# Performance work log

Hardware: AMD Instinct MI355X
Metric: run time of the kernel (lower is better)

The kernel has to match this reference:

```python
import jax, jax.numpy as jnp
import numpy as np

N_ROUTING_ITERS = 10


def setup_inputs() -> dict:
    key = jax.random.key(0)
    k1, k2, k3 = jax.random.split(key, 3)
    b, in_caps, in_ch, out_ch = 64, 1152, 512, 512
    input_x = jax.random.normal(k1, (b, in_caps, in_ch), dtype=jnp.float32)
    # nn.Linear(in_ch, out_ch): weight [out, in] -> store transposed [in, out]
    lim = 1.0 / np.sqrt(in_ch)
    W = jax.random.uniform(k2, (in_ch, out_ch), minval=-lim, maxval=lim, dtype=jnp.float32)
    bias = jax.random.uniform(k3, (out_ch,), minval=-lim, maxval=lim, dtype=jnp.float32)
    coeffs = jnp.ones((1, in_caps, 1), dtype=jnp.float32)
    return {"input_x": input_x, "W": W, "bias": bias, "coeffs": coeffs}


def _squash(sj):
    # squash over channel dim: x * ||x||^2 / ((1+||x||^2) * ||x||) = x * ||x|| / (1+||x||^2)
    norm = jnp.linalg.norm(sj, axis=-1, keepdims=True)
    return sj * norm / (1.0 + norm * norm)


def reference(input_x, W, bias, coeffs):
    # u_ji: [b, in_caps, out_ch]
    u = jnp.einsum('bic,co->bio', input_x, W) + bias

    def step(c, _):
        cij = jax.nn.softmax(c, axis=1)                      # [1, in_caps, 1]
        sj = jnp.sum(u * cij, axis=1, keepdims=True)         # [b, 1, out]
        vj = _squash(sj).squeeze(1)                          # [b, out]
        upd = jnp.einsum('bio,bo->i', u, vj)                 # agreement, summed over batch
        return c + upd[None, :, None], vj

    _, vjs = jax.lax.scan(step, coeffs, None, length=N_ROUTING_ITERS)
    return vjs[-1]
```

## Files before the change

### kernel.cpp

```cpp
#include <hip/hip_runtime.h>
#include <cstddef>

#define B      64
#define IC     1152
#define CH     512
#define SPLITS 16


__device__ __forceinline__ float waveReduceSum(float v) {
    #pragma unroll
    for (int o = 32; o; o >>= 1) v += __shfl_down(v, o, 64);
    return v;
}
__device__ __forceinline__ float waveReduceMax(float v) {
    #pragma unroll
    for (int o = 32; o; o >>= 1) v = fmaxf(v, __shfl_down(v, o, 64));
    return v;
}

template<int NT>
__device__ __forceinline__ float blockReduceSum(float v, float* red) {
    __syncthreads();
    const int lane = threadIdx.x & 63, w = threadIdx.x >> 6;
    v = waveReduceSum(v);
    if (lane == 0) red[w] = v;
    __syncthreads();
    if (threadIdx.x == 0) {
        float t = red[0];
        #pragma unroll
        for (int k = 1; k < NT / 64; ++k) t += red[k];
        red[0] = t;
    }
    __syncthreads();
    return red[0];
}

template<int NT>
__device__ __forceinline__ float blockReduceMax(float v, float* red) {
    __syncthreads();
    const int lane = threadIdx.x & 63, w = threadIdx.x >> 6;
    v = waveReduceMax(v);
    if (lane == 0) red[w] = v;
    __syncthreads();
    if (threadIdx.x == 0) {
        float t = red[0];
        #pragma unroll
        for (int k = 1; k < NT / 64; ++k) t = fmaxf(t, red[k]);
        red[0] = t;
    }
    __syncthreads();
    return red[0];
}


__global__ __launch_bounds__(1024) void k_transpose(const float* __restrict__ W,
                                                    float* __restrict__ WT) {
    __shared__ float tile[32][33];
    int x = blockIdx.x * 32 + threadIdx.x;
    int y = blockIdx.y * 32 + threadIdx.y;
    tile[threadIdx.y][threadIdx.x] = W[(size_t)y * CH + x];
    __syncthreads();
    int tx = blockIdx.y * 32 + threadIdx.x;
    int ty = blockIdx.x * 32 + threadIdx.y;
    WT[(size_t)ty * CH + tx] = tile[threadIdx.x][threadIdx.y];
}

__global__ __launch_bounds__(256) void k_wwt(const float* __restrict__ W,
                                             const float* __restrict__ WT,
                                             float* __restrict__ WWT) {
    __shared__ float wa[2][CH];
    const int a0 = blockIdx.x * 2;
    for (int j = threadIdx.x; j < CH; j += 256) {
        wa[0][j] = W[(size_t)a0 * CH + j];
        wa[1][j] = W[(size_t)(a0 + 1) * CH + j];
    }
    __syncthreads();
    const int c0 = threadIdx.x, c1 = threadIdx.x + 256;
    float a00 = 0, a01 = 0, a10 = 0, a11 = 0;
    for (int j = 0; j < CH; ++j) {
        float w0 = wa[0][j], w1 = wa[1][j];
        float t0 = WT[(size_t)j * CH + c0], t1 = WT[(size_t)j * CH + c1];
        a00 += w0 * t0; a01 += w0 * t1;
        a10 += w1 * t0; a11 += w1 * t1;
    }
    WWT[(size_t)a0 * CH + c0] = a00;
    WWT[(size_t)a0 * CH + c1] = a01;
    WWT[(size_t)(a0 + 1) * CH + c0] = a10;
    WWT[(size_t)(a0 + 1) * CH + c1] = a11;
}

__global__ __launch_bounds__(512) void k_wb(const float* __restrict__ WT,
                                            const float* __restrict__ bias,
                                            float* __restrict__ Wb,
                                            float* __restrict__ bb) {
    __shared__ float bS[CH];
    __shared__ float red[8];
    const int c = threadIdx.x;
    bS[c] = bias[c];
    __syncthreads();
    float acc = 0;
    for (int j = 0; j < CH; ++j) acc += bS[j] * WT[(size_t)j * CH + c];
    Wb[c] = acc;
    float n2 = blockReduceSum<512>(bS[c] * bS[c], red);
    if (c == 0) *bb = n2;
}

__global__ void k_init(const float* __restrict__ coeffs, float* __restrict__ cvec) {
    int i = blockIdx.x * 256 + threadIdx.x;
    if (i < IC) cvec[i] = coeffs[i];
}


__global__ __launch_bounds__(256) void k_passA(const float* __restrict__ x,
                                               const float* __restrict__ cvec,
                                               float* __restrict__ xcpart) {
    __shared__ float eS[IC];
    __shared__ float red[4];
    const int b = blockIdx.x, is = blockIdx.y;
    const int t = threadIdx.x;

    float cl[5];
    float m = -3.4e38f;
    #pragma unroll
    for (int k = 0; k < 5; ++k) {
        int i = t + k * 256;
        cl[k] = (i < IC) ? cvec[i] : -3.4e38f;
        m = fmaxf(m, cl[k]);
    }
    float M = blockReduceMax<256>(m, red);
    float z = 0;
    #pragma unroll
    for (int k = 0; k < 5; ++k) {
        int i = t + k * 256;
        if (i < IC) { float e = expf(cl[k] - M); eS[i] = e; z += e; }
    }
    float Z = blockReduceSum<256>(z, red);
    const float invZ = 1.0f / Z;

    const int i0 = is * (IC / SPLITS);
    float2 acc = make_float2(0.f, 0.f);
    const float2* xp = reinterpret_cast<const float2*>(x + ((size_t)b * IC + i0) * CH) + t;
    #pragma unroll 4
    for (int i = i0; i < i0 + IC / SPLITS; ++i) {
        float w = eS[i];
        float2 xv = *xp;
        acc.x += w * xv.x;
        acc.y += w * xv.y;
        xp += CH / 2;
    }
    float2* outp = reinterpret_cast<float2*>(xcpart + ((size_t)(is * B + b)) * CH) + t;
    *outp = make_float2(acc.x * invZ, acc.y * invZ);
}

__global__ __launch_bounds__(1024) void k_core(const float* __restrict__ xcpart,
                                               const float* __restrict__ WWT,
                                               const float* __restrict__ Wb,
                                               const float* __restrict__ bbp,
                                               float* __restrict__ Wv) {
    __shared__ float xcS[CH];
    __shared__ float hS[CH];
    __shared__ float red[16];
    __shared__ float gS;
    const int b = blockIdx.x, tid = threadIdx.x;
    const int c = tid & (CH - 1), half = tid >> 9;

    if (half == 0) {
        float s = 0;
        #pragma unroll
        for (int is = 0; is < SPLITS; ++is) s += xcpart[((size_t)(is * B + b)) * CH + c];
        xcS[c] = s;
    }
    __syncthreads();

    float acc = 0;
    const int cp0 = half * (CH / 2);
    for (int cp = cp0; cp < cp0 + CH / 2; ++cp)
        acc += xcS[cp] * WWT[(size_t)cp * CH + c];
    if (half == 0) hS[c] = acc;
    __syncthreads();
    if (half == 1) hS[c] += acc;
    __syncthreads();

    float part = 0;
    if (half == 0) {
        float xcv = xcS[c];
        part = xcv * hS[c] + 2.0f * Wb[c] * xcv;
    }
    float tot = blockReduceSum<1024>(part, red);
    if (tid == 0) {
        float n2 = tot + *bbp;
        float n = sqrtf(n2);
        gS = n / (1.0f + n2);
    }
    __syncthreads();
    if (half == 0) Wv[(size_t)b * CH + c] = gS * (hS[c] + Wb[c]);
}

__global__ __launch_bounds__(256) void k_passC(const float* __restrict__ x,
                                               const float* __restrict__ Wv,
                                               float* __restrict__ cvec) {
    __shared__ float red[4];
    const int i = blockIdx.x, t = threadIdx.x;
    float acc = 0;
    const float2* wvp = reinterpret_cast<const float2*>(Wv) + t;
    const float2* xp = reinterpret_cast<const float2*>(x) + (size_t)i * (CH / 2) + t;
    #pragma unroll 4
    for (int b = 0; b < B; ++b) {
        float2 xv = xp[(size_t)b * IC * (CH / 2)];
        float2 wv = wvp[(size_t)b * (CH / 2)];
        acc += xv.x * wv.x + xv.y * wv.y;
    }
    float tot = blockReduceSum<256>(acc, red);
    if (t == 0) cvec[i] += tot;
}

__global__ __launch_bounds__(512) void k_final(const float* __restrict__ xcpart,
                                               const float* __restrict__ W,
                                               const float* __restrict__ bias,
                                               float* __restrict__ out) {
    __shared__ float xcS[CH];
    __shared__ float red[8];
    __shared__ float gS;
    const int b = blockIdx.x, j = threadIdx.x;
    float s = 0;
    #pragma unroll
    for (int is = 0; is < SPLITS; ++is) s += xcpart[((size_t)(is * B + b)) * CH + j];
    xcS[j] = s;
    __syncthreads();
    float sj = bias[j];
    for (int c = 0; c < CH; ++c) sj += xcS[c] * W[(size_t)c * CH + j];
    float n2 = blockReduceSum<512>(sj * sj, red);
    if (j == 0) { float n = sqrtf(n2); gS = n / (1.0f + n2); }
    __syncthreads();
    out[(size_t)b * CH + j] = sj * gS;
}


extern "C" void kernel_launch(void* const* d_in, const int* in_sizes, int n_in,
                              void* d_out, int out_size, void* d_ws, size_t ws_size,
                              hipStream_t stream) {
    (void)in_sizes; (void)n_in; (void)out_size; (void)ws_size;
    const float* x      = (const float*)d_in[0];
    const float* W      = (const float*)d_in[1];
    const float* bias   = (const float*)d_in[2];
    const float* coeffs = (const float*)d_in[3];
    float* out = (float*)d_out;
    float* ws  = (float*)d_ws;

    float* WT     = ws;
    float* WWT    = ws + 262144;
    float* Wb     = ws + 524288;
    float* bb     = ws + 524800;
    float* cvec   = ws + 524816;
    float* Wv     = ws + 525968;
    float* xcpart = ws + 558736;

    k_transpose<<<dim3(16, 16), dim3(32, 32), 0, stream>>>(W, WT);
    k_wwt<<<256, 256, 0, stream>>>(W, WT, WWT);
    k_wb<<<1, 512, 0, stream>>>(WT, bias, Wb, bb);
    k_init<<<5, 256, 0, stream>>>(coeffs, cvec);

    for (int t = 0; t < 9; ++t) {
        k_passA<<<dim3(B, SPLITS), 256, 0, stream>>>(x, cvec, xcpart);
        k_core<<<B, 1024, 0, stream>>>(xcpart, WWT, Wb, bb, Wv);
        k_passC<<<IC, 256, 0, stream>>>(x, Wv, cvec);
    }
    k_passA<<<dim3(B, SPLITS), 256, 0, stream>>>(x, cvec, xcpart);
    k_final<<<B, 512, 0, stream>>>(xcpart, W, bias, out);
}
```

Baseline: 1.275 ms.

## Convert input to bf16 once and stream it in routing passes

```diff
diff --git a/kernel.cpp b/kernel.cpp
--- a/kernel.cpp
+++ b/kernel.cpp
@@ -52,6 +52,30 @@
     return red[0];
 }
 
+__device__ __forceinline__ unsigned bfpack2(float a, float b) {
+    unsigned ua = __float_as_uint(a), ub = __float_as_uint(b);
+    ua = (ua + 0x7FFFu + ((ua >> 16) & 1u)) >> 16;
+    ub = (ub + 0x7FFFu + ((ub >> 16) & 1u)) & 0xFFFF0000u;
+    return ua | ub;
+}
+__device__ __forceinline__ void bfunpack2(unsigned u, float& lo, float& hi) {
+    lo = __uint_as_float(u << 16);
+    hi = __uint_as_float(u & 0xFFFF0000u);
+}
+
+
+__global__ __launch_bounds__(1024) void k_cvt(const float* __restrict__ x,
+                                              uint4* __restrict__ xbf) {
+    const size_t idx = (size_t)blockIdx.x * 1024 + threadIdx.x;
+    const float4* xp = reinterpret_cast<const float4*>(x) + idx * 2;
+    float4 a = xp[0], b = xp[1];
+    uint4 o;
+    o.x = bfpack2(a.x, a.y);
+    o.y = bfpack2(a.z, a.w);
+    o.z = bfpack2(b.x, b.y);
+    o.w = bfpack2(b.z, b.w);
+    xbf[idx] = o;
+}
 
 __global__ __launch_bounds__(1024) void k_transpose(const float* __restrict__ W,
                                                     float* __restrict__ WT) {
@@ -111,10 +135,11 @@
 }
 
 
-__global__ __launch_bounds__(256) void k_passA(const float* __restrict__ x,
+__global__ __launch_bounds__(256) void k_passA(const uint4* __restrict__ xbf,
                                                const float* __restrict__ cvec,
                                                float* __restrict__ xcpart) {
     __shared__ float eS[IC];
+    __shared__ float accS[3][CH];
     __shared__ float red[4];
     const int b = blockIdx.x, is = blockIdx.y;
     const int t = threadIdx.x;
@@ -137,19 +162,42 @@
     float Z = blockReduceSum<256>(z, red);
     const float invZ = 1.0f / Z;
 
+    const int rp = t >> 6;
+    const int c8 = t & 63;
     const int i0 = is * (IC / SPLITS);
-    float2 acc = make_float2(0.f, 0.f);
-    const float2* xp = reinterpret_cast<const float2*>(x + ((size_t)b * IC + i0) * CH) + t;
-    #pragma unroll 4
-    for (int i = i0; i < i0 + IC / SPLITS; ++i) {
-        float w = eS[i];
-        float2 xv = *xp;
-        acc.x += w * xv.x;
-        acc.y += w * xv.y;
-        xp += CH / 2;
-    }
-    float2* outp = reinterpret_cast<float2*>(xcpart + ((size_t)(is * B + b)) * CH) + t;
-    *outp = make_float2(acc.x * invZ, acc.y * invZ);
+
+    float acc[8];
+    #pragma unroll
+    for (int e = 0; e < 8; ++e) acc[e] = 0.f;
+
+    const uint4* xp = xbf + ((size_t)(b * IC + i0 + rp) * (CH / 8)) + c8;
+    #pragma unroll 2
+    for (int k = 0; k < IC / SPLITS / 4; ++k) {
+        float w = eS[i0 + rp + 4 * k];
+        uint4 u = xp[(size_t)k * 4 * (CH / 8)];
+        float f0, f1;
+        bfunpack2(u.x, f0, f1); acc[0] += w * f0; acc[1] += w * f1;
+        bfunpack2(u.y, f0, f1); acc[2] += w * f0; acc[3] += w * f1;
+        bfunpack2(u.z, f0, f1); acc[4] += w * f0; acc[5] += w * f1;
+        bfunpack2(u.w, f0, f1); acc[6] += w * f0; acc[7] += w * f1;
+    }
+    if (rp > 0) {
+        #pragma unroll
+        for (int e = 0; e < 8; ++e) accS[rp - 1][c8 * 8 + e] = acc[e];
+    }
+    __syncthreads();
+    if (rp == 0) {
+        float4 o0, o1;
+        #pragma unroll
+        for (int e = 0; e < 8; ++e) {
+            float v = acc[e] + accS[0][c8 * 8 + e] + accS[1][c8 * 8 + e] + accS[2][c8 * 8 + e];
+            if (e < 4) reinterpret_cast<float*>(&o0)[e] = v * invZ;
+            else       reinterpret_cast<float*>(&o1)[e - 4] = v * invZ;
+        }
+        float4* outp = reinterpret_cast<float4*>(xcpart + ((size_t)(is * B + b)) * CH) + c8 * 2;
+        outp[0] = o0;
+        outp[1] = o1;
+    }
 }
 
 __global__ __launch_bounds__(1024) void k_core(const float* __restrict__ xcpart,
@@ -196,9 +244,76 @@
     if (half == 0) Wv[(size_t)b * CH + c] = gS * (hS[c] + Wb[c]);
 }
 
-__global__ __launch_bounds__(256) void k_passC(const float* __restrict__ x,
+__global__ __launch_bounds__(256) void k_passC(const uint4* __restrict__ xbf,
                                                const float* __restrict__ Wv,
                                                float* __restrict__ cvec) {
+    __shared__ float red[4];
+    const int i = blockIdx.x, t = threadIdx.x;
+    const int bp = t >> 6;
+    const int c8 = t & 63;
+
+    float acc = 0;
+    #pragma unroll 2
+    for (int k = 0; k < B / 4; ++k) {
+        int b = bp + 4 * k;
+        uint4 u = xbf[((size_t)(b * IC + i)) * (CH / 8) + c8];
+        const float4* wvp = reinterpret_cast<const float4*>(Wv + (size_t)b * CH) + c8 * 2;
+        float4 w0 = wvp[0], w1 = wvp[1];
+        float f0, f1;
+        bfunpack2(u.x, f0, f1); acc += f0 * w0.x + f1 * w0.y;
+        bfunpack2(u.y, f0, f1); acc += f0 * w0.z + f1 * w0.w;
+        bfunpack2(u.z, f0, f1); acc += f0 * w1.x + f1 * w1.y;
+        bfunpack2(u.w, f0, f1); acc += f0 * w1.z + f1 * w1.w;
+    }
+    float tot = blockReduceSum<256>(acc, red);
+    if (t == 0) cvec[i] += tot;
+}
+
+
+__global__ __launch_bounds__(256) void k_passA_f32(const float* __restrict__ x,
+                                                   const float* __restrict__ cvec,
+                                                   float* __restrict__ xcpart) {
+    __shared__ float eS[IC];
+    __shared__ float red[4];
+    const int b = blockIdx.x, is = blockIdx.y;
+    const int t = threadIdx.x;
+
+    float cl[5];
+    float m = -3.4e38f;
+    #pragma unroll
+    for (int k = 0; k < 5; ++k) {
+        int i = t + k * 256;
+        cl[k] = (i < IC) ? cvec[i] : -3.4e38f;
+        m = fmaxf(m, cl[k]);
+    }
+    float M = blockReduceMax<256>(m, red);
+    float z = 0;
+    #pragma unroll
+    for (int k = 0; k < 5; ++k) {
+        int i = t + k * 256;
+        if (i < IC) { float e = expf(cl[k] - M); eS[i] = e; z += e; }
+    }
+    float Z = blockReduceSum<256>(z, red);
+    const float invZ = 1.0f / Z;
+
+    const int i0 = is * (IC / SPLITS);
+    float2 acc = make_float2(0.f, 0.f);
+    const float2* xp = reinterpret_cast<const float2*>(x + ((size_t)b * IC + i0) * CH) + t;
+    #pragma unroll 4
+    for (int i = i0; i < i0 + IC / SPLITS; ++i) {
+        float w = eS[i];
+        float2 xv = *xp;
+        acc.x += w * xv.x;
+        acc.y += w * xv.y;
+        xp += CH / 2;
+    }
+    float2* outp = reinterpret_cast<float2*>(xcpart + ((size_t)(is * B + b)) * CH) + t;
+    *outp = make_float2(acc.x * invZ, acc.y * invZ);
+}
+
+__global__ __launch_bounds__(256) void k_passC_f32(const float* __restrict__ x,
+                                                   const float* __restrict__ Wv,
+                                                   float* __restrict__ cvec) {
     __shared__ float red[4];
     const int i = blockIdx.x, t = threadIdx.x;
     float acc = 0;
@@ -239,13 +354,19 @@
 extern "C" void kernel_launch(void* const* d_in, const int* in_sizes, int n_in,
                               void* d_out, int out_size, void* d_ws, size_t ws_size,
                               hipStream_t stream) {
-    (void)in_sizes; (void)n_in; (void)out_size; (void)ws_size;
+    (void)in_sizes; (void)n_in; (void)out_size;
     const float* x      = (const float*)d_in[0];
     const float* W      = (const float*)d_in[1];
     const float* bias   = (const float*)d_in[2];
     const float* coeffs = (const float*)d_in[3];
     float* out = (float*)d_out;
-    float* ws  = (float*)d_ws;
+
+    const size_t xbf_bytes  = (size_t)B * IC * CH * 2;
+    const size_t f32_floats = 1083024;
+    const bool fast = ws_size >= xbf_bytes + f32_floats * 4 + 256;
+
+    uint4* xbf = (uint4*)d_ws;
+    float* ws  = fast ? (float*)((char*)d_ws + xbf_bytes) : (float*)d_ws;
 
     float* WT     = ws;
     float* WWT    = ws + 262144;
@@ -255,16 +376,27 @@
     float* Wv     = ws + 525968;
     float* xcpart = ws + 558736;
 
+    if (fast)
+        k_cvt<<<(B * IC * CH / 8) / 1024, 1024, 0, stream>>>(x, xbf);
     k_transpose<<<dim3(16, 16), dim3(32, 32), 0, stream>>>(W, WT);
     k_wwt<<<256, 256, 0, stream>>>(W, WT, WWT);
     k_wb<<<1, 512, 0, stream>>>(WT, bias, Wb, bb);
     k_init<<<5, 256, 0, stream>>>(coeffs, cvec);
 
     for (int t = 0; t < 9; ++t) {
-        k_passA<<<dim3(B, SPLITS), 256, 0, stream>>>(x, cvec, xcpart);
-        k_core<<<B, 1024, 0, stream>>>(xcpart, WWT, Wb, bb, Wv);
-        k_passC<<<IC, 256, 0, stream>>>(x, Wv, cvec);
-    }
-    k_passA<<<dim3(B, SPLITS), 256, 0, stream>>>(x, cvec, xcpart);
+        if (fast) {
+            k_passA<<<dim3(B, SPLITS), 256, 0, stream>>>(xbf, cvec, xcpart);
+            k_core<<<B, 1024, 0, stream>>>(xcpart, WWT, Wb, bb, Wv);
+            k_passC<<<IC, 256, 0, stream>>>(xbf, Wv, cvec);
+        } else {
+            k_passA_f32<<<dim3(B, SPLITS), 256, 0, stream>>>(x, cvec, xcpart);
+            k_core<<<B, 1024, 0, stream>>>(xcpart, WWT, Wb, bb, Wv);
+            k_passC_f32<<<IC, 256, 0, stream>>>(x, Wv, cvec);
+        }
+    }
+    if (fast)
+        k_passA<<<dim3(B, SPLITS), 256, 0, stream>>>(xbf, cvec, xcpart);
+    else
+        k_passA_f32<<<dim3(B, SPLITS), 256, 0, stream>>>(x, cvec, xcpart);
     k_final<<<B, 512, 0, stream>>>(xcpart, W, bias, out);
 }
```

After: 1.117 ms. -12.4%, faster.

## Fuse routing iteration into one kernel over a bf16 copy of x

Applied to the files above, without the earlier changes.

```diff
diff --git a/kernel.cpp b/kernel.cpp
--- a/kernel.cpp
+++ b/kernel.cpp
@@ -4,7 +4,7 @@
 #define B      64
 #define IC     1152
 #define CH     512
-#define SPLITS 16
+#define NCVT   2048
 
 
 __device__ __forceinline__ float waveReduceSum(float v) {
@@ -18,7 +18,7 @@
     return v;
 }
 
-template<int NT>
+template<int NTT>
 __device__ __forceinline__ float blockReduceSum(float v, float* red) {
     __syncthreads();
     const int lane = threadIdx.x & 63, w = threadIdx.x >> 6;
@@ -28,14 +28,14 @@
     if (threadIdx.x == 0) {
         float t = red[0];
         #pragma unroll
-        for (int k = 1; k < NT / 64; ++k) t += red[k];
+        for (int k = 1; k < NTT / 64; ++k) t += red[k];
         red[0] = t;
     }
     __syncthreads();
     return red[0];
 }
 
-template<int NT>
+template<int NTT>
 __device__ __forceinline__ float blockReduceMax(float v, float* red) {
     __syncthreads();
     const int lane = threadIdx.x & 63, w = threadIdx.x >> 6;
@@ -45,13 +45,260 @@
     if (threadIdx.x == 0) {
         float t = red[0];
         #pragma unroll
-        for (int k = 1; k < NT / 64; ++k) t = fmaxf(t, red[k]);
+        for (int k = 1; k < NTT / 64; ++k) t = fmaxf(t, red[k]);
         red[0] = t;
     }
     __syncthreads();
     return red[0];
 }
 
+__device__ __forceinline__ unsigned bfpack2(float a, float b) {
+    unsigned ua = __float_as_uint(a), ub = __float_as_uint(b);
+    ua = (ua + 0x7FFFu + ((ua >> 16) & 1u)) >> 16;
+    ub = (ub + 0x7FFFu + ((ub >> 16) & 1u)) & 0xFFFF0000u;
+    return ua | ub;
+}
+__device__ __forceinline__ void bfunpack2(unsigned u, float& lo, float& hi) {
+    lo = __uint_as_float(u << 16);
+    hi = __uint_as_float(u & 0xFFFF0000u);
+}
+
+
+__global__ __launch_bounds__(256) void k_setup(
+    const float* __restrict__ x, const float* __restrict__ W,
+    const float* __restrict__ bias, const float* __restrict__ coeffs,
+    uint4* __restrict__ xbf, float* __restrict__ WWT, float* __restrict__ Wb,
+    float* __restrict__ bb, float* __restrict__ bufs)
+{
+    __shared__ float red[4];
+    const int bid = blockIdx.x, tid = threadIdx.x;
+
+    if (bid < NCVT) {
+        const size_t base = (size_t)bid * (256 * 9) + tid;
+        const float4* xp4 = reinterpret_cast<const float4*>(x);
+        #pragma unroll 3
+        for (int k = 0; k < 9; ++k) {
+            size_t idx = base + (size_t)k * 256;
+            float4 a = xp4[idx * 2], b2 = xp4[idx * 2 + 1];
+            uint4 o;
+            o.x = bfpack2(a.x, a.y); o.y = bfpack2(a.z, a.w);
+            o.z = bfpack2(b2.x, b2.y); o.w = bfpack2(b2.z, b2.w);
+            xbf[idx] = o;
+        }
+    } else if (bid < NCVT + 1024) {
+        const int bidw = bid - NCVT;
+        const int ta = bidw >> 5, tc = bidw & 31;
+        const int a = ta * 16 + (tid >> 4), c2 = tc * 16 + (tid & 15);
+        const float* ra = W + (size_t)a * CH;
+        const float* rc = W + (size_t)c2 * CH;
+        float s = 0;
+        for (int j = 0; j < CH; ++j) s += ra[j] * rc[j];
+        WWT[(size_t)a * CH + c2] = s;
+    } else if (bid == NCVT + 1024) {
+        #pragma unroll
+        for (int r = 0; r < 2; ++r) {
+            int c = tid + r * 256;
+            const float* rw = W + (size_t)c * CH;
+            float s = 0;
+            for (int j = 0; j < CH; ++j) s += rw[j] * bias[j];
+            Wb[c] = s;
+        }
+    } else if (bid == NCVT + 1025) {
+        float v0 = bias[tid], v1 = bias[tid + 256];
+        float n2 = blockReduceSum<256>(v0 * v0 + v1 * v1, red);
+        if (tid == 0) *bb = n2;
+    } else {
+        for (int i = tid; i < IC; i += 256) bufs[i] = coeffs[i];
+        for (int k = tid; k < 9 * IC; k += 256) bufs[IC + k] = 0.f;
+    }
+}
+
+
+__global__ __launch_bounds__(1024) void k_iter(
+    const uint4* __restrict__ xbf, const float* __restrict__ WWT,
+    const float* __restrict__ Wb, const float* __restrict__ bbp,
+    const float* __restrict__ cin, float* __restrict__ cout)
+{
+    __shared__ float eS[IC];
+    __shared__ float accS[15][CH];
+    __shared__ float xcS[CH];
+    __shared__ float hS[CH];
+    __shared__ float WvS[CH];
+    __shared__ float red[16];
+    __shared__ float gS;
+    const int b = blockIdx.x, tid = threadIdx.x;
+
+    float c0v = cin[tid];
+    float c1v = (tid < IC - 1024) ? cin[tid + 1024] : -3.4e38f;
+    float M = blockReduceMax<1024>(fmaxf(c0v, c1v), red);
+    float e0 = expf(c0v - M);
+    float e1 = (tid < IC - 1024) ? expf(c1v - M) : 0.f;
+    eS[tid] = e0;
+    if (tid < IC - 1024) eS[tid + 1024] = e1;
+    float Z = blockReduceSum<1024>(e0 + e1, red);
+    const float invZ = 1.0f / Z;
+
+    const int rp = tid >> 6;
+    const int c8 = tid & 63;
+    float acc[8];
+    #pragma unroll
+    for (int e = 0; e < 8; ++e) acc[e] = 0.f;
+    {
+        const uint4* xp = xbf + ((size_t)b * IC + rp) * (CH / 8) + c8;
+        for (int i = rp; i < IC; i += 16) {
+            float w = eS[i];
+            uint4 u = *xp; xp += 16 * (CH / 8);
+            float f0, f1;
+            bfunpack2(u.x, f0, f1); acc[0] += w * f0; acc[1] += w * f1;
+            bfunpack2(u.y, f0, f1); acc[2] += w * f0; acc[3] += w * f1;
+            bfunpack2(u.z, f0, f1); acc[4] += w * f0; acc[5] += w * f1;
+            bfunpack2(u.w, f0, f1); acc[6] += w * f0; acc[7] += w * f1;
+        }
+    }
+    if (rp > 0) {
+        #pragma unroll
+        for (int e = 0; e < 8; ++e) accS[rp - 1][c8 * 8 + e] = acc[e];
+    }
+    __syncthreads();
+    if (rp == 0) {
+        #pragma unroll
+        for (int e = 0; e < 8; ++e) {
+            float v = acc[e];
+            #pragma unroll
+            for (int k = 0; k < 15; ++k) v += accS[k][c8 * 8 + e];
+            xcS[c8 * 8 + e] = v * invZ;
+        }
+    }
+    __syncthreads();
+
+    const int cc = tid & (CH - 1), half = tid >> 9;
+    float hp = 0;
+    {
+        const int cp0 = half * (CH / 2);
+        for (int cp = cp0; cp < cp0 + CH / 2; ++cp)
+            hp += xcS[cp] * WWT[(size_t)cp * CH + cc];
+    }
+    if (half == 1) hS[cc] = hp;
+    __syncthreads();
+    float part = 0;
+    if (half == 0) {
+        float h = hp + hS[cc];
+        hS[cc] = h;
+        float xv = xcS[cc];
+        part = xv * h + 2.0f * Wb[cc] * xv;
+    }
+    float tot = blockReduceSum<1024>(part, red);
+    if (tid == 0) {
+        float n2 = tot + *bbp;
+        float n = sqrtf(n2);
+        gS = n / (1.0f + n2);
+    }
+    __syncthreads();
+    if (half == 0) WvS[cc] = gS * (hS[cc] + Wb[cc]);
+    __syncthreads();
+
+    {
+        const float4* wv4 = reinterpret_cast<const float4*>(WvS) + c8 * 2;
+        float4 w0 = wv4[0], w1 = wv4[1];
+        const uint4* xq = xbf + ((size_t)b * IC + rp) * (CH / 8) + c8;
+        for (int i = rp; i < IC; i += 16) {
+            uint4 u = *xq; xq += 16 * (CH / 8);
+            float f0, f1, s = 0;
+            bfunpack2(u.x, f0, f1); s += f0 * w0.x + f1 * w0.y;
+            bfunpack2(u.y, f0, f1); s += f0 * w0.z + f1 * w0.w;
+            bfunpack2(u.z, f0, f1); s += f0 * w1.x + f1 * w1.y;
+            bfunpack2(u.w, f0, f1); s += f0 * w1.z + f1 * w1.w;
+            s = waveReduceSum(s);
+            if (c8 == 0) atomicAdd(cout + i, s);
+        }
+    }
+    if (b == 0) {
+        for (int i = tid; i < IC; i += 1024) atomicAdd(cout + i, cin[i]);
+    }
+}
+
+
+__global__ __launch_bounds__(1024) void k_final(
+    const uint4* __restrict__ xbf, const float* __restrict__ W,
+    const float* __restrict__ bias, const float* __restrict__ cin,
+    float* __restrict__ out)
+{
+    __shared__ float eS[IC];
+    __shared__ float accS[15][CH];
+    __shared__ float xcS[CH];
+    __shared__ float hS[CH];
+    __shared__ float red[16];
+    __shared__ float gS;
+    const int b = blockIdx.x, tid = threadIdx.x;
+
+    float c0v = cin[tid];
+    float c1v = (tid < IC - 1024) ? cin[tid + 1024] : -3.4e38f;
+    float M = blockReduceMax<1024>(fmaxf(c0v, c1v), red);
+    float e0 = expf(c0v - M);
+    float e1 = (tid < IC - 1024) ? expf(c1v - M) : 0.f;
+    eS[tid] = e0;
+    if (tid < IC - 1024) eS[tid + 1024] = e1;
+    float Z = blockReduceSum<1024>(e0 + e1, red);
+    const float invZ = 1.0f / Z;
+
+    const int rp = tid >> 6, c8 = tid & 63;
+    float acc[8];
+    #pragma unroll
+    for (int e = 0; e < 8; ++e) acc[e] = 0.f;
+    {
+        const uint4* xp = xbf + ((size_t)b * IC + rp) * (CH / 8) + c8;
+        for (int i = rp; i < IC; i += 16) {
+            float w = eS[i];
+            uint4 u = *xp; xp += 16 * (CH / 8);
+            float f0, f1;
+            bfunpack2(u.x, f0, f1); acc[0] += w * f0; acc[1] += w * f1;
+            bfunpack2(u.y, f0, f1); acc[2] += w * f0; acc[3] += w * f1;
+            bfunpack2(u.z, f0, f1); acc[4] += w * f0; acc[5] += w * f1;
+            bfunpack2(u.w, f0, f1); acc[6] += w * f0; acc[7] += w * f1;
+        }
+    }
+    if (rp > 0) {
+        #pragma unroll
+        for (int e = 0; e < 8; ++e) accS[rp - 1][c8 * 8 + e] = acc[e];
+    }
+    __syncthreads();
+    if (rp == 0) {
+        #pragma unroll
+        for (int e = 0; e < 8; ++e) {
+            float v = acc[e];
+            #pragma unroll
+            for (int k = 0; k < 15; ++k) v += accS[k][c8 * 8 + e];
+            xcS[c8 * 8 + e] = v * invZ;
+        }
+    }
+    __syncthreads();
+
+    const int j = tid & (CH - 1), half = tid >> 9;
+    float sp = 0;
+    {
+        const int cp0 = half * (CH / 2);
+        for (int cp = cp0; cp < cp0 + CH / 2; ++cp)
+            sp += xcS[cp] * W[(size_t)cp * CH + j];
+    }
+    if (half == 1) hS[j] = sp;
+    __syncthreads();
+    float part = 0;
+    if (half == 0) {
+        float s = sp + hS[j] + bias[j];
+        hS[j] = s;
+        part = s * s;
+    }
+    float tot = blockReduceSum<1024>(part, red);
+    if (tid == 0) {
+        float n = sqrtf(tot);
+        gS = n / (1.0f + tot);
+    }
+    __syncthreads();
+    if (half == 0) out[(size_t)b * CH + j] = hS[j] * gS;
+}
+
+
+#define SPLITS 16
 
 __global__ __launch_bounds__(1024) void k_transpose(const float* __restrict__ W,
                                                     float* __restrict__ WT) {
@@ -65,9 +312,9 @@
     WT[(size_t)ty * CH + tx] = tile[threadIdx.x][threadIdx.y];
 }
 
-__global__ __launch_bounds__(256) void k_wwt(const float* __restrict__ W,
-                                             const float* __restrict__ WT,
-                                             float* __restrict__ WWT) {
+__global__ __launch_bounds__(256) void k_wwt_f(const float* __restrict__ W,
+                                               const float* __restrict__ WT,
+                                               float* __restrict__ WWT) {
     __shared__ float wa[2][CH];
     const int a0 = blockIdx.x * 2;
     for (int j = threadIdx.x; j < CH; j += 256) {
@@ -89,10 +336,10 @@
     WWT[(size_t)(a0 + 1) * CH + c1] = a11;
 }
 
-__global__ __launch_bounds__(512) void k_wb(const float* __restrict__ WT,
-                                            const float* __restrict__ bias,
-                                            float* __restrict__ Wb,
-                                            float* __restrict__ bb) {
+__global__ __launch_bounds__(512) void k_wb_f(const float* __restrict__ WT,
+                                              const float* __restrict__ bias,
+                                              float* __restrict__ Wb,
+                                              float* __restrict__ bb) {
     __shared__ float bS[CH];
     __shared__ float red[8];
     const int c = threadIdx.x;
@@ -105,20 +352,18 @@
     if (c == 0) *bb = n2;
 }
 
-__global__ void k_init(const float* __restrict__ coeffs, float* __restrict__ cvec) {
+__global__ void k_init_f(const float* __restrict__ coeffs, float* __restrict__ cvec) {
     int i = blockIdx.x * 256 + threadIdx.x;
     if (i < IC) cvec[i] = coeffs[i];
 }
 
-
-__global__ __launch_bounds__(256) void k_passA(const float* __restrict__ x,
-                                               const float* __restrict__ cvec,
-                                               float* __restrict__ xcpart) {
+__global__ __launch_bounds__(256) void k_passA_f32(const float* __restrict__ x,
+                                                   const float* __restrict__ cvec,
+                                                   float* __restrict__ xcpart) {
     __shared__ float eS[IC];
     __shared__ float red[4];
     const int b = blockIdx.x, is = blockIdx.y;
     const int t = threadIdx.x;
-
     float cl[5];
     float m = -3.4e38f;
     #pragma unroll
@@ -136,7 +381,6 @@
     }
     float Z = blockReduceSum<256>(z, red);
     const float invZ = 1.0f / Z;
-
     const int i0 = is * (IC / SPLITS);
     float2 acc = make_float2(0.f, 0.f);
     const float2* xp = reinterpret_cast<const float2*>(x + ((size_t)b * IC + i0) * CH) + t;
@@ -152,18 +396,17 @@
     *outp = make_float2(acc.x * invZ, acc.y * invZ);
 }
 
-__global__ __launch_bounds__(1024) void k_core(const float* __restrict__ xcpart,
-                                               const float* __restrict__ WWT,
-                                               const float* __restrict__ Wb,
-                                               const float* __restrict__ bbp,
-                                               float* __restrict__ Wv) {
+__global__ __launch_bounds__(1024) void k_core_f(const float* __restrict__ xcpart,
+                                                 const float* __restrict__ WWT,
+                                                 const float* __restrict__ Wb,
+                                                 const float* __restrict__ bbp,
+                                                 float* __restrict__ Wv) {
     __shared__ float xcS[CH];
     __shared__ float hS[CH];
     __shared__ float red[16];
     __shared__ float gS;
     const int b = blockIdx.x, tid = threadIdx.x;
     const int c = tid & (CH - 1), half = tid >> 9;
-
     if (half == 0) {
         float s = 0;
         #pragma unroll
@@ -171,7 +414,6 @@
         xcS[c] = s;
     }
     __syncthreads();
-
     float acc = 0;
     const int cp0 = half * (CH / 2);
     for (int cp = cp0; cp < cp0 + CH / 2; ++cp)
@@ -180,7 +422,6 @@
     __syncthreads();
     if (half == 1) hS[c] += acc;
     __syncthreads();
-
     float part = 0;
     if (half == 0) {
         float xcv = xcS[c];
@@ -196,9 +437,9 @@
     if (half == 0) Wv[(size_t)b * CH + c] = gS * (hS[c] + Wb[c]);
 }
 
-__global__ __launch_bounds__(256) void k_passC(const float* __restrict__ x,
-                                               const float* __restrict__ Wv,
-                                               float* __restrict__ cvec) {
+__global__ __launch_bounds__(256) void k_passC_f32(const float* __restrict__ x,
+                                                   const float* __restrict__ Wv,
+                                                   float* __restrict__ cvec) {
     __shared__ float red[4];
     const int i = blockIdx.x, t = threadIdx.x;
     float acc = 0;
@@ -214,10 +455,10 @@
     if (t == 0) cvec[i] += tot;
 }
 
-__global__ __launch_bounds__(512) void k_final(const float* __restrict__ xcpart,
-                                               const float* __restrict__ W,
-                                               const float* __restrict__ bias,
-                                               float* __restrict__ out) {
+__global__ __launch_bounds__(512) void k_final_f(const float* __restrict__ xcpart,
+                                                 const float* __restrict__ W,
+                                                 const float* __restrict__ bias,
+                                                 float* __restrict__ out) {
     __shared__ float xcS[CH];
     __shared__ float red[8];
     __shared__ float gS;
@@ -239,32 +480,52 @@
 extern "C" void kernel_launch(void* const* d_in, const int* in_sizes, int n_in,
                               void* d_out, int out_size, void* d_ws, size_t ws_size,
                               hipStream_t stream) {
-    (void)in_sizes; (void)n_in; (void)out_size; (void)ws_size;
+    (void)in_sizes; (void)n_in; (void)out_size;
     const float* x      = (const float*)d_in[0];
     const float* W      = (const float*)d_in[1];
     const float* bias   = (const float*)d_in[2];
     const float* coeffs = (const float*)d_in[3];
     float* out = (float*)d_out;
-    float* ws  = (float*)d_ws;
-
-    float* WT     = ws;
-    float* WWT    = ws + 262144;
-    float* Wb     = ws + 524288;
-    float* bb     = ws + 524800;
-    float* cvec   = ws + 524816;
-    float* Wv     = ws + 525968;
-    float* xcpart = ws + 558736;
-
-    k_transpose<<<dim3(16, 16), dim3(32, 32), 0, stream>>>(W, WT);
-    k_wwt<<<256, 256, 0, stream>>>(W, WT, WWT);
-    k_wb<<<1, 512, 0, stream>>>(WT, bias, Wb, bb);
-    k_init<<<5, 256, 0, stream>>>(coeffs, cvec);
-
-    for (int t = 0; t < 9; ++t) {
-        k_passA<<<dim3(B, SPLITS), 256, 0, stream>>>(x, cvec, xcpart);
-        k_core<<<B, 1024, 0, stream>>>(xcpart, WWT, Wb, bb, Wv);
-        k_passC<<<IC, 256, 0, stream>>>(x, Wv, cvec);
-    }
-    k_passA<<<dim3(B, SPLITS), 256, 0, stream>>>(x, cvec, xcpart);
-    k_final<<<B, 512, 0, stream>>>(xcpart, W, bias, out);
-}
+
+    const size_t xbf_bytes = (size_t)B * IC * CH * 2;
+    const size_t fast_floats = 262144 + 512 + 16 + 10 * IC + 64;
+    const bool fast = ws_size >= xbf_bytes + fast_floats * 4 + 256;
+
+    if (fast) {
+        uint4* xbf = (uint4*)d_ws;
+        float* ws  = (float*)((char*)d_ws + xbf_bytes);
+        float* WWT  = ws;
+        float* Wb   = ws + 262144;
+        float* bb   = ws + 262656;
+        float* bufs = ws + 262672;
+
+        k_setup<<<NCVT + 1024 + 3, 256, 0, stream>>>(x, W, bias, coeffs,
+                                                     xbf, WWT, Wb, bb, bufs);
+        for (int t = 0; t < 9; ++t)
+            k_iter<<<B, 1024, 0, stream>>>(xbf, WWT, Wb, bb,
+                                           bufs + (size_t)t * IC,
+                                           bufs + (size_t)(t + 1) * IC);
+        k_final<<<B, 1024, 0, stream>>>(xbf, W, bias, bufs + (size_t)9 * IC, out);
+    } else {
+        float* ws = (float*)d_ws;
+        float* WT     = ws;
+        float* WWT    = ws + 262144;
+        float* Wb     = ws + 524288;
+        float* bb     = ws + 524800;
+        float* cvec   = ws + 524816;
+        float* Wv     = ws + 525968;
+        float* xcpart = ws + 558736;
+
+        k_transpose<<<dim3(16, 16), dim3(32, 32), 0, stream>>>(W, WT);
+        k_wwt_f<<<256, 256, 0, stream>>>(W, WT, WWT);
+        k_wb_f<<<1, 512, 0, stream>>>(WT, bias, Wb, bb);
+        k_init_f<<<5, 256, 0, stream>>>(coeffs, cvec);
+        for (int t = 0; t < 9; ++t) {
+            k_passA_f32<<<dim3(B, SPLITS), 256, 0, stream>>>(x, cvec, xcpart);
+            k_core_f<<<B, 1024, 0, stream>>>(xcpart, WWT, Wb, bb, Wv);
+            k_passC_f32<<<IC, 256, 0, stream>>>(x, Wv, cvec);
+        }
+        k_passA_f32<<<dim3(B, SPLITS), 256, 0, stream>>>(x, cvec, xcpart);
+        k_final_f<<<B, 512, 0, stream>>>(xcpart, W, bias, out);
+    }
+}
```

New measurement: 2.009 ms. 1.58x slower.
